# Kernel optimization log

Measured on AMD Instinct MI355X. Metric: run time of the kernel, lower is better.

The kernel has to match this reference:

```python
import jax, jax.numpy as jnp
import numpy as np

B, T, D = 8, 1024, 1024
F = 4 * D  # RWKV channel-mixing hidden size
EPS = 1e-3  # keras LayerNormalization default epsilon


def layer_norm(x, g, b):
    mu = jnp.mean(x, axis=-1, keepdims=True)
    var = jnp.var(x, axis=-1, keepdims=True)
    return (x - mu) * jax.lax.rsqrt(var + EPS) * g + b


def setup_inputs() -> dict:
    key = jax.random.key(0)
    ks = jax.random.split(key, 16)
    s = 0.02
    f32 = jnp.float32
    return {
        "x": jax.random.normal(ks[0], (B, T, D), f32),
        "att_x": jnp.zeros((B, D), f32),
        "att_a": jnp.zeros((B, D), f32),
        "att_b": jnp.zeros((B, D), f32),
        "att_p": jnp.zeros((B, D), f32),
        "ffn_x": jnp.zeros((B, D), f32),
        "ln1_g": jnp.ones((D,), f32),
        "ln1_b": jnp.zeros((D,), f32),
        "ln2_g": jnp.ones((D,), f32),
        "ln2_b": jnp.zeros((D,), f32),
        "tm_mix_k": jax.random.uniform(ks[1], (D,), f32),
        "tm_mix_v": jax.random.uniform(ks[2], (D,), f32),
        "tm_mix_r": jax.random.uniform(ks[3], (D,), f32),
        "tm_decay": jax.random.normal(ks[4], (D,), f32) * 0.1,
        "tm_first": jax.random.normal(ks[5], (D,), f32) * 0.1,
        "Wk": jax.random.normal(ks[6], (D, D), f32) * s,
        "Wv": jax.random.normal(ks[7], (D, D), f32) * s,
        "Wr": jax.random.normal(ks[8], (D, D), f32) * s,
        "Wo": jax.random.normal(ks[9], (D, D), f32) * s,
        "cm_mix_k": jax.random.uniform(ks[10], (D,), f32),
        "cm_mix_r": jax.random.uniform(ks[11], (D,), f32),
        "Ck": jax.random.normal(ks[12], (D, F), f32) * s,
        "Cr": jax.random.normal(ks[13], (D, D), f32) * s,
        "Cv": jax.random.normal(ks[14], (F, D), f32) * s,
    }


def _wkv_scan(k, v, aa, bb, pp, decay, first):
    # k, v: [B, T, D]; states: [B, D]. Numerically-stable RWKV-4 WKV recurrence.
    w = -jnp.exp(decay)  # per-channel decay, always negative

    def step(carry, kv):
        aa, bb, pp = carry
        k_t, v_t = kv
        ww = first + k_t
        p = jnp.maximum(pp, ww)
        e1 = jnp.exp(pp - p)
        e2 = jnp.exp(ww - p)
        wkv = (e1 * aa + e2 * v_t) / (e1 * bb + e2)
        ww2 = pp + w
        p2 = jnp.maximum(ww2, k_t)
        e1b = jnp.exp(ww2 - p2)
        e2b = jnp.exp(k_t - p2)
        return (e1b * aa + e2b * v_t, e1b * bb + e2b, p2), wkv

    kT = jnp.swapaxes(k, 0, 1)  # [T, B, D]
    vT = jnp.swapaxes(v, 0, 1)
    (aa, bb, pp), wkv = jax.lax.scan(step, (aa, bb, pp), (kT, vT))
    return jnp.swapaxes(wkv, 0, 1), aa, bb, pp


def reference(x, att_x, att_a, att_b, att_p, ffn_x,
              ln1_g, ln1_b, ln2_g, ln2_b,
              tm_mix_k, tm_mix_v, tm_mix_r, tm_decay, tm_first,
              Wk, Wv, Wr, Wo, cm_mix_k, cm_mix_r, Ck, Cr, Cv):
    # ---- time mixing (RWKV attention) on ln1(x) ----
    xn = layer_norm(x, ln1_g, ln1_b)  # [B, T, D]
    x_prev = jnp.concatenate([att_x[:, None, :], xn[:, :-1, :]], axis=1)  # token shift
    k = (xn * tm_mix_k + x_prev * (1.0 - tm_mix_k)) @ Wk
    v = (xn * tm_mix_v + x_prev * (1.0 - tm_mix_v)) @ Wv
    r = jax.nn.sigmoid((xn * tm_mix_r + x_prev * (1.0 - tm_mix_r)) @ Wr)
    wkv, aa, bb, pp = _wkv_scan(k, v, att_a, att_b, att_p, tm_decay, tm_first)
    x1 = x + (r * wkv) @ Wo  # residual

    # ---- channel mixing (FFN) on ln2(x1) ----
    xn2 = layer_norm(x1, ln2_g, ln2_b)
    xp = jnp.concatenate([ffn_x[:, None, :], xn2[:, :-1, :]], axis=1)
    kc = jnp.square(jax.nn.relu((xn2 * cm_mix_k + xp * (1.0 - cm_mix_k)) @ Ck))
    rc = jax.nn.sigmoid((xn2 * cm_mix_r + xp * (1.0 - cm_mix_r)) @ Cr)
    out = x1 + rc * (kc @ Cv)

    return (out, xn[:, -1, :], aa, bb, pp, xn2[:, -1, :])
```

## Files before the change

### kernel.cpp

```cpp
#include <hip/hip_runtime.h>

#define TT 1024
#define DD 1024
#define BB 8
#define FF 4096
#define MM (BB * TT)
#define CHL 32
#define NCH (TT / CHL)
#define NCHAN (BB * DD)

typedef unsigned short u16;
typedef unsigned int u32;

typedef __attribute__((ext_vector_type(8))) short short8;
typedef __attribute__((ext_vector_type(4))) float floatx4;

__device__ __forceinline__ u16 f2bf(float f) {
  u32 u = __float_as_uint(f);
  u32 r = (u + 0x7fffu + ((u >> 16) & 1u)) >> 16;
  return (u16)r;
}
__device__ __forceinline__ float bf2f(u16 h) { return __uint_as_float(((u32)h) << 16); }
__device__ __forceinline__ float sigmoidf_(float v) { return 1.0f / (1.0f + __expf(-v)); }

__global__ void transpose5_bf16(const float* __restrict__ w0, const float* __restrict__ w1,
                                const float* __restrict__ w2, const float* __restrict__ w3,
                                const float* __restrict__ w4, u16* __restrict__ outbase) {
  __shared__ float tile[32][33];
  const float* srcs[5] = {w0, w1, w2, w3, w4};
  const float* in = srcs[blockIdx.z];
  u16* out = outbase + (size_t)blockIdx.z * 1024 * 1024;
  int tx = threadIdx.x, ty = threadIdx.y;
  int n0 = blockIdx.x * 32, k0 = blockIdx.y * 32;
#pragma unroll
  for (int j = 0; j < 32; j += 8)
    tile[ty + j][tx] = in[(size_t)(k0 + ty + j) * 1024 + (n0 + tx)];
  __syncthreads();
#pragma unroll
  for (int j = 0; j < 32; j += 8)
    out[(size_t)(n0 + ty + j) * 1024 + (k0 + tx)] = f2bf(tile[tx][ty + j]);
}

__global__ void transpose_bf16(const float* __restrict__ in, u16* __restrict__ out, int K, int N) {
  __shared__ float tile[32][33];
  int tx = threadIdx.x, ty = threadIdx.y;
  int n0 = blockIdx.x * 32, k0 = blockIdx.y * 32;
#pragma unroll
  for (int j = 0; j < 32; j += 8)
    tile[ty + j][tx] = in[(size_t)(k0 + ty + j) * N + (n0 + tx)];
  __syncthreads();
#pragma unroll
  for (int j = 0; j < 32; j += 8)
    out[(size_t)(n0 + ty + j) * K + (k0 + tx)] = f2bf(tile[tx][ty + j]);
}

__global__ void ln1mix_kernel(const float* __restrict__ x, const float* __restrict__ attx,
                              const float* __restrict__ g, const float* __restrict__ be,
                              const float* __restrict__ mk, const float* __restrict__ mv,
                              const float* __restrict__ mr,
                              u16* __restrict__ xk, u16* __restrict__ xv, u16* __restrict__ xr,
                              float* __restrict__ xn_last) {
  int row = blockIdx.x, tid = threadIdx.x;
  int b = row >> 10, t = row & (TT - 1);
  float4 xc = ((const float4*)(x + (size_t)row * DD))[tid];
  float4 xp = (t == 0) ? ((const float4*)(attx + (size_t)b * DD))[tid]
                       : ((const float4*)(x + (size_t)(row - 1) * DD))[tid];
  float sc = xc.x + xc.y + xc.z + xc.w;
  float qc = xc.x * xc.x + xc.y * xc.y + xc.z * xc.z + xc.w * xc.w;
  float sp = xp.x + xp.y + xp.z + xp.w;
  float qp = xp.x * xp.x + xp.y * xp.y + xp.z * xp.z + xp.w * xp.w;
#pragma unroll
  for (int o = 32; o > 0; o >>= 1) {
    sc += __shfl_xor(sc, o); qc += __shfl_xor(qc, o);
    sp += __shfl_xor(sp, o); qp += __shfl_xor(qp, o);
  }
  __shared__ float red[4][4];
  int lane = tid & 63, wid = tid >> 6;
  if (lane == 0) { red[wid][0] = sc; red[wid][1] = qc; red[wid][2] = sp; red[wid][3] = qp; }
  __syncthreads();
  sc = red[0][0] + red[1][0] + red[2][0] + red[3][0];
  qc = red[0][1] + red[1][1] + red[2][1] + red[3][1];
  sp = red[0][2] + red[1][2] + red[2][2] + red[3][2];
  qp = red[0][3] + red[1][3] + red[2][3] + red[3][3];
  const float inv = 1.0f / (float)DD;
  float muc = sc * inv, varc = qc * inv - muc * muc;
  float rc = rsqrtf(varc + 1e-3f);
  float mup = sp * inv, varp = qp * inv - mup * mup;
  float rp = rsqrtf(varp + 1e-3f);
  float4 gg = ((const float4*)g)[tid];
  float4 bb = ((const float4*)be)[tid];
  float4 k4 = ((const float4*)mk)[tid];
  float4 v4 = ((const float4*)mv)[tid];
  float4 r4 = ((const float4*)mr)[tid];
  float xcv[4] = {xc.x, xc.y, xc.z, xc.w};
  float xpv[4] = {xp.x, xp.y, xp.z, xp.w};
  float gv[4] = {gg.x, gg.y, gg.z, gg.w};
  float bv[4] = {bb.x, bb.y, bb.z, bb.w};
  float kv[4] = {k4.x, k4.y, k4.z, k4.w};
  float vv[4] = {v4.x, v4.y, v4.z, v4.w};
  float rv[4] = {r4.x, r4.y, r4.z, r4.w};
  u16 ok[4], ov[4], orr[4];
  float nc[4];
#pragma unroll
  for (int i = 0; i < 4; i++) {
    nc[i] = (xcv[i] - muc) * rc * gv[i] + bv[i];
    float np = (t == 0) ? xpv[i] : ((xpv[i] - mup) * rp * gv[i] + bv[i]);
    ok[i] = f2bf(nc[i] * kv[i] + np * (1.0f - kv[i]));
    ov[i] = f2bf(nc[i] * vv[i] + np * (1.0f - vv[i]));
    orr[i] = f2bf(nc[i] * rv[i] + np * (1.0f - rv[i]));
  }
  size_t o4 = (size_t)row * (DD / 4) + tid;
  ((ushort4*)xk)[o4] = make_ushort4(ok[0], ok[1], ok[2], ok[3]);
  ((ushort4*)xv)[o4] = make_ushort4(ov[0], ov[1], ov[2], ov[3]);
  ((ushort4*)xr)[o4] = make_ushort4(orr[0], orr[1], orr[2], orr[3]);
  if (t == TT - 1)
    ((float4*)xn_last)[(size_t)b * (DD / 4) + tid] = make_float4(nc[0], nc[1], nc[2], nc[3]);
}

__global__ void ln2mix_kernel(const float* __restrict__ x1, const float* __restrict__ ffnx,
                              const float* __restrict__ g, const float* __restrict__ be,
                              const float* __restrict__ cmk, const float* __restrict__ cmr,
                              u16* __restrict__ xk2, u16* __restrict__ xr2,
                              float* __restrict__ xn2_last) {
  int row = blockIdx.x, tid = threadIdx.x;
  int b = row >> 10, t = row & (TT - 1);
  float4 xc = ((const float4*)(x1 + (size_t)row * DD))[tid];
  float4 xp = (t == 0) ? ((const float4*)(ffnx + (size_t)b * DD))[tid]
                       : ((const float4*)(x1 + (size_t)(row - 1) * DD))[tid];
  float sc = xc.x + xc.y + xc.z + xc.w;
  float qc = xc.x * xc.x + xc.y * xc.y + xc.z * xc.z + xc.w * xc.w;
  float sp = xp.x + xp.y + xp.z + xp.w;
  float qp = xp.x * xp.x + xp.y * xp.y + xp.z * xp.z + xp.w * xp.w;
#pragma unroll
  for (int o = 32; o > 0; o >>= 1) {
    sc += __shfl_xor(sc, o); qc += __shfl_xor(qc, o);
    sp += __shfl_xor(sp, o); qp += __shfl_xor(qp, o);
  }
  __shared__ float red[4][4];
  int lane = tid & 63, wid = tid >> 6;
  if (lane == 0) { red[wid][0] = sc; red[wid][1] = qc; red[wid][2] = sp; red[wid][3] = qp; }
  __syncthreads();
  sc = red[0][0] + red[1][0] + red[2][0] + red[3][0];
  qc = red[0][1] + red[1][1] + red[2][1] + red[3][1];
  sp = red[0][2] + red[1][2] + red[2][2] + red[3][2];
  qp = red[0][3] + red[1][3] + red[2][3] + red[3][3];
  const float inv = 1.0f / (float)DD;
  float muc = sc * inv, varc = qc * inv - muc * muc;
  float rc = rsqrtf(varc + 1e-3f);
  float mup = sp * inv, varp = qp * inv - mup * mup;
  float rp = rsqrtf(varp + 1e-3f);
  float4 gg = ((const float4*)g)[tid];
  float4 bb = ((const float4*)be)[tid];
  float4 k4 = ((const float4*)cmk)[tid];
  float4 r4 = ((const float4*)cmr)[tid];
  float xcv[4] = {xc.x, xc.y, xc.z, xc.w};
  float xpv[4] = {xp.x, xp.y, xp.z, xp.w};
  float gv[4] = {gg.x, gg.y, gg.z, gg.w};
  float bv[4] = {bb.x, bb.y, bb.z, bb.w};
  float kv[4] = {k4.x, k4.y, k4.z, k4.w};
  float rv[4] = {r4.x, r4.y, r4.z, r4.w};
  u16 ok[4], orr[4];
  float nc[4];
#pragma unroll
  for (int i = 0; i < 4; i++) {
    nc[i] = (xcv[i] - muc) * rc * gv[i] + bv[i];
    float np = (t == 0) ? xpv[i] : ((xpv[i] - mup) * rp * gv[i] + bv[i]);
    ok[i] = f2bf(nc[i] * kv[i] + np * (1.0f - kv[i]));
    orr[i] = f2bf(nc[i] * rv[i] + np * (1.0f - rv[i]));
  }
  size_t o4 = (size_t)row * (DD / 4) + tid;
  ((ushort4*)xk2)[o4] = make_ushort4(ok[0], ok[1], ok[2], ok[3]);
  ((ushort4*)xr2)[o4] = make_ushort4(orr[0], orr[1], orr[2], orr[3]);
  if (t == TT - 1)
    ((float4*)xn2_last)[(size_t)b * (DD / 4) + tid] = make_float4(nc[0], nc[1], nc[2], nc[3]);
}

__global__ void wkv_chunk_sum(const float* __restrict__ K, const float* __restrict__ V,
                              const float* __restrict__ decay,
                              float* __restrict__ sa, float* __restrict__ sb,
                              float* __restrict__ ps) {
  int f = blockIdx.x * 256 + threadIdx.x;
  int d = f & (DD - 1);
  int bc = f >> 10;
  int b = bc & (BB - 1);
  int chunk = bc >> 3;
  float w = -__expf(decay[d]);
  const float* kp = K + ((size_t)(b * TT + chunk * CHL)) * DD + d;
  const float* vp = V + ((size_t)(b * TT + chunk * CHL)) * DD + d;
  float aa = 0.0f, bb = 0.0f, pp = -1e30f;
#pragma unroll
  for (int j = 0; j < CHL; j++) {
    float kt = kp[(size_t)j * DD];
    float vt = vp[(size_t)j * DD];
    float ww2 = pp + w;
    float p2 = fmaxf(ww2, kt);
    float e1 = __expf(ww2 - p2);
    float e2 = __expf(kt - p2);
    aa = e1 * aa + e2 * vt;
    bb = e1 * bb + e2;
    pp = p2;
  }
  int ch = b * DD + d;
  size_t s = (size_t)chunk * NCHAN + ch;
  sa[s] = aa; sb[s] = bb; ps[s] = pp;
}

__global__ void wkv_chunk_scan(const float* __restrict__ sa, const float* __restrict__ sb,
                               const float* __restrict__ ps, const float* __restrict__ decay,
                               const float* __restrict__ aa0, const float* __restrict__ bb0,
                               const float* __restrict__ pp0,
                               float* __restrict__ pa, float* __restrict__ pb,
                               float* __restrict__ ppx,
                               float* __restrict__ aa_out, float* __restrict__ bb_out,
                               float* __restrict__ pp_out) {
  int ch = blockIdx.x * 256 + threadIdx.x;
  int d = ch & (DD - 1);
  float w = -__expf(decay[d]);
  float wL = (float)CHL * w;
  float aa = aa0[ch], bb = bb0[ch], pp = pp0[ch];
  float lsa[NCH], lsb[NCH], lps[NCH];
#pragma unroll
  for (int j = 0; j < NCH; j++) {
    size_t s = (size_t)j * NCHAN + ch;
    lsa[j] = sa[s]; lsb[j] = sb[s]; lps[j] = ps[s];
  }
#pragma unroll
  for (int j = 0; j < NCH; j++) {
    size_t s = (size_t)j * NCHAN + ch;
    pa[s] = aa; pb[s] = bb; ppx[s] = pp;
    float pw = pp + wL;
    float pn = fmaxf(pw, lps[j]);
    float e1 = __expf(pw - pn);
    float e2 = __expf(lps[j] - pn);
    aa = e1 * aa + e2 * lsa[j];
    bb = e1 * bb + e2 * lsb[j];
    pp = pn;
  }
  aa_out[ch] = aa; bb_out[ch] = bb; pp_out[ch] = pp;
}

__global__ void wkv_chunk_out(const float* __restrict__ K, const float* __restrict__ V,
                              const u16* __restrict__ sigr, const float* __restrict__ decay,
                              const float* __restrict__ first,
                              const float* __restrict__ pa, const float* __restrict__ pb,
                              const float* __restrict__ ppx, u16* __restrict__ rm) {
  int f = blockIdx.x * 256 + threadIdx.x;
  int d = f & (DD - 1);
  int bc = f >> 10;
  int b = bc & (BB - 1);
  int chunk = bc >> 3;
  float w = -__expf(decay[d]);
  float u = first[d];
  int ch = b * DD + d;
  size_t s = (size_t)chunk * NCHAN + ch;
  float aa = pa[s], bb = pb[s], pp = ppx[s];
  size_t base = ((size_t)(b * TT + chunk * CHL)) * DD + d;
  const float* kp = K + base;
  const float* vp = V + base;
  const u16* rp = sigr + base;
  u16* op = rm + base;
#pragma unroll
  for (int j = 0; j < CHL; j++) {
    float kt = kp[(size_t)j * DD];
    float vt = vp[(size_t)j * DD];
    float ww = u + kt;
    float p = fmaxf(pp, ww);
    float e1 = __expf(pp - p);
    float e2 = __expf(ww - p);
    float wkv = __fdividef(e1 * aa + e2 * vt, e1 * bb + e2);
    op[(size_t)j * DD] = f2bf(bf2f(rp[(size_t)j * DD]) * wkv);
    float ww2 = pp + w;
    float p2 = fmaxf(ww2, kt);
    float e1b = __expf(ww2 - p2);
    float e2b = __expf(kt - p2);
    aa = e1b * aa + e2b * vt;
    bb = e1b * bb + e2b;
    pp = p2;
  }
}


template <int MODE>
__launch_bounds__(256, 3)
__global__ void gemm_bt(const u16* __restrict__ A0, const u16* __restrict__ BT0,
                        const float* R1, const u16* R2,
                        void* C0, void* C1, void* C2, int M, int N, int K) {
  __shared__ u16 lA[128 * 64];
  __shared__ u16 lB[128 * 64];
  int tid = threadIdx.x;
  int lane = tid & 63;
  int wid = tid >> 6;
  int wy = wid >> 1, wx = wid & 1;

  const u16* A = A0;
  const u16* BT = BT0;
  void* Cout = C0;
  if (MODE == 5) {
    int z = blockIdx.z;
    A = A0 + (size_t)z * M * K;
    BT = BT0 + (size_t)z * N * K;
    Cout = (z == 0) ? C0 : (z == 1) ? C1 : C2;
  }

  int bx = blockIdx.x, by = blockIdx.y;
  {
    int flat = by * gridDim.x + bx;
    int j = flat >> 3;
    by = (flat & 7) * 8 + (j & 7);
    bx = j >> 3;
  }
  int m0 = by * 128, n0 = bx * 128;

  int rlo = lane & 15;
  int rr = tid >> 3;
  int cc = ((tid & 7) - rr) & 7;
  const u16* gA = A + (size_t)(m0 + rr) * K + cc * 8;
  const u16* gB = BT + (size_t)(n0 + rr) * K + cc * 8;
  u16* ldsA = lA + wid * 512;
  u16* ldsB = lB + wid * 512;
  size_t qstep = (size_t)32 * K;

  floatx4 acc[4][4];
#pragma unroll
  for (int mi = 0; mi < 4; mi++)
#pragma unroll
    for (int ni = 0; ni < 4; ni++)
#pragma unroll
      for (int e = 0; e < 4; e++) acc[mi][ni][e] = 0.0f;

  for (int kt = 0; kt < K; kt += 64) {
    __syncthreads();
#pragma unroll
    for (int q = 0; q < 4; q++) {
      __builtin_amdgcn_global_load_lds(gA + q * qstep + kt, ldsA + q * 2048, 16, 0, 0);
      __builtin_amdgcn_global_load_lds(gB + q * qstep + kt, ldsB + q * 2048, 16, 0, 0);
    }
    __syncthreads();
    short8 af[2][4], bfr[2][4];
#pragma unroll
    for (int s = 0; s < 2; s++) {
      int cbase = s * 4 + (lane >> 4);
#pragma unroll
      for (int mi = 0; mi < 4; mi++) {
        int row = wy * 64 + mi * 16 + rlo;
        af[s][mi] = *(const short8*)&lA[row * 64 + (((cbase + row) & 7) << 3)];
      }
#pragma unroll
      for (int ni = 0; ni < 4; ni++) {
        int row = wx * 64 + ni * 16 + rlo;
        bfr[s][ni] = *(const short8*)&lB[row * 64 + (((cbase + row) & 7) << 3)];
      }
    }
#pragma unroll
    for (int s = 0; s < 2; s++)
#pragma unroll
      for (int mi = 0; mi < 4; mi++)
#pragma unroll
        for (int ni = 0; ni < 4; ni++)
          acc[mi][ni] =
              __builtin_amdgcn_mfma_f32_16x16x32_bf16(af[s][mi], bfr[s][ni], acc[mi][ni], 0, 0, 0);
  }

  int rbase = (lane >> 4) * 4;
#pragma unroll
  for (int mi = 0; mi < 4; mi++) {
#pragma unroll
    for (int ni = 0; ni < 4; ni++) {
#pragma unroll
      for (int r = 0; r < 4; r++) {
        int row = m0 + wy * 64 + mi * 16 + rbase + r;
        int col = n0 + wx * 64 + ni * 16 + rlo;
        size_t idx = (size_t)row * N + col;
        float v = acc[mi][ni][r];
        if (MODE == 0) {
          ((float*)Cout)[idx] = v;
        } else if (MODE == 1) {
          ((u16*)Cout)[idx] = f2bf(sigmoidf_(v));
        } else if (MODE == 2) {
          float tpos = fmaxf(v, 0.0f);
          ((u16*)Cout)[idx] = f2bf(tpos * tpos);
        } else if (MODE == 3) {
          ((float*)Cout)[idx] = v + R1[idx];
        } else if (MODE == 4) {
          ((float*)Cout)[idx] = R1[idx] + bf2f(R2[idx]) * v;
        } else {
          if (blockIdx.z == 2)
            ((u16*)Cout)[idx] = f2bf(sigmoidf_(v));
          else
            ((float*)Cout)[idx] = v;
        }
      }
    }
  }
}

extern "C" void kernel_launch(void* const* d_in, const int* in_sizes, int n_in,
                              void* d_out, int out_size, void* d_ws, size_t ws_size,
                              hipStream_t stream) {
  const float* x    = (const float*)d_in[0];
  const float* attx = (const float*)d_in[1];
  const float* aa0  = (const float*)d_in[2];
  const float* bb0  = (const float*)d_in[3];
  const float* pp0  = (const float*)d_in[4];
  const float* ffnx = (const float*)d_in[5];
  const float* ln1g = (const float*)d_in[6];
  const float* ln1b = (const float*)d_in[7];
  const float* ln2g = (const float*)d_in[8];
  const float* ln2b = (const float*)d_in[9];
  const float* mk   = (const float*)d_in[10];
  const float* mv   = (const float*)d_in[11];
  const float* mr   = (const float*)d_in[12];
  const float* decay= (const float*)d_in[13];
  const float* first= (const float*)d_in[14];
  const float* Wk   = (const float*)d_in[15];
  const float* Wv   = (const float*)d_in[16];
  const float* Wr   = (const float*)d_in[17];
  const float* Wo   = (const float*)d_in[18];
  const float* cmk  = (const float*)d_in[19];
  const float* cmr  = (const float*)d_in[20];
  const float* Ck   = (const float*)d_in[21];
  const float* Cr   = (const float*)d_in[22];
  const float* Cv   = (const float*)d_in[23];

  float* out      = (float*)d_out;
  float* xn_last  = out + (size_t)BB * TT * DD;
  float* aa_out   = xn_last + BB * DD;
  float* bb_out   = aa_out + BB * DD;
  float* pp_out   = bb_out + BB * DD;
  float* xn2_last = pp_out + BB * DD;
  float* x1 = out;

  char* ws = (char*)d_ws;
  const size_t MB = 1024ull * 1024ull;
  u16* WT5   = (u16*)(ws + 0 * MB);
  u16* WkT   = WT5;
  u16* WoT   = (u16*)(ws + 6 * MB);
  u16* CrT   = (u16*)(ws + 8 * MB);
  u16* CkT   = (u16*)(ws + 10 * MB);
  u16* CvT   = (u16*)(ws + 18 * MB);
  u16* xk    = (u16*)(ws + 26 * MB);
  u16* xv    = (u16*)(ws + 42 * MB);
  u16* xr    = (u16*)(ws + 58 * MB);
  float* kbuf= (float*)(ws + 74 * MB);
  float* vbuf= (float*)(ws + 106 * MB);
  u16* sigr  = (u16*)(ws + 138 * MB);
  float* sab = (float*)(ws + 154 * MB);
  float* sbb = (float*)(ws + 155 * MB);
  float* psb = (float*)(ws + 156 * MB);
  float* pab = (float*)(ws + 157 * MB);
  float* pbb = (float*)(ws + 158 * MB);
  float* ppb = (float*)(ws + 159 * MB);
  u16* rmb   = (u16*)(ws + 26 * MB);
  u16* xk2   = (u16*)(ws + 26 * MB);
  u16* xr2   = (u16*)(ws + 42 * MB);
  u16* sigr2 = (u16*)(ws + 58 * MB);
  u16* kc    = (u16*)(ws + 74 * MB);

  dim3 tb32(32, 8);
  transpose5_bf16<<<dim3(32, 32, 5), tb32, 0, stream>>>(Wk, Wv, Wr, Wo, Cr, WT5);
  transpose_bf16<<<dim3(128, 32), tb32, 0, stream>>>(Ck, CkT, 1024, 4096);
  transpose_bf16<<<dim3(32, 128), tb32, 0, stream>>>(Cv, CvT, 4096, 1024);

  ln1mix_kernel<<<MM, 256, 0, stream>>>(x, attx, ln1g, ln1b, mk, mv, mr, xk, xv, xr, xn_last);

  gemm_bt<5><<<dim3(8, 64, 3), 256, 0, stream>>>(xk, WkT, nullptr, nullptr,
                                                 kbuf, vbuf, sigr, MM, 1024, 1024);

  wkv_chunk_sum<<<NCHAN * NCH / 256, 256, 0, stream>>>(kbuf, vbuf, decay, sab, sbb, psb);
  wkv_chunk_scan<<<NCHAN / 256, 256, 0, stream>>>(sab, sbb, psb, decay, aa0, bb0, pp0,
                                                  pab, pbb, ppb, aa_out, bb_out, pp_out);
  wkv_chunk_out<<<NCHAN * NCH / 256, 256, 0, stream>>>(kbuf, vbuf, sigr, decay, first,
                                                       pab, pbb, ppb, rmb);

  gemm_bt<3><<<dim3(8, 64), 256, 0, stream>>>(rmb, WoT, x, nullptr, x1, nullptr, nullptr,
                                              MM, 1024, 1024);

  ln2mix_kernel<<<MM, 256, 0, stream>>>(x1, ffnx, ln2g, ln2b, cmk, cmr, xk2, xr2, xn2_last);

  gemm_bt<2><<<dim3(32, 64), 256, 0, stream>>>(xk2, CkT, nullptr, nullptr, kc, nullptr, nullptr,
                                               MM, 4096, 1024);
  gemm_bt<1><<<dim3(8, 64), 256, 0, stream>>>(xr2, CrT, nullptr, nullptr, sigr2, nullptr, nullptr,
                                              MM, 1024, 1024);
  gemm_bt<4><<<dim3(8, 64), 256, 0, stream>>>(kc, CvT, x1, sigr2, out, nullptr, nullptr,
                                              MM, 1024, 4096);
}
```

Measured before the change: 511.8 us.

## Store k/v in bf16 and fuse Ck and Cr GEMMs into one launch

The projection GEMM now writes k and v as bf16 instead of fp32, halving the traffic the WKV chunk kernels read. The Ck and Cr channel-mix GEMMs merge into one launch over a concatenated transposed weight buffer, and each block picks its A matrix and epilogue by column range. Launch bounds rise to 4 blocks per SM to raise occupancy. The cost is lower precision on k/v before the exponential recurrence, and possible register pressure from the tighter bounds.

New measurement: 502.8 us. No clear change (-1.8%).

```diff
diff --git a/kernel.cpp b/kernel.cpp
--- a/kernel.cpp
+++ b/kernel.cpp
@@ -25,11 +25,12 @@
 
 __global__ void transpose5_bf16(const float* __restrict__ w0, const float* __restrict__ w1,
                                 const float* __restrict__ w2, const float* __restrict__ w3,
-                                const float* __restrict__ w4, u16* __restrict__ outbase) {
+                                const float* __restrict__ w4,
+                                u16* __restrict__ out4, u16* __restrict__ crdst) {
   __shared__ float tile[32][33];
   const float* srcs[5] = {w0, w1, w2, w3, w4};
   const float* in = srcs[blockIdx.z];
-  u16* out = outbase + (size_t)blockIdx.z * 1024 * 1024;
+  u16* out = (blockIdx.z == 4) ? crdst : out4 + (size_t)blockIdx.z * 1024 * 1024;
   int tx = threadIdx.x, ty = threadIdx.y;
   int n0 = blockIdx.x * 32, k0 = blockIdx.y * 32;
 #pragma unroll
@@ -175,7 +176,7 @@
     ((float4*)xn2_last)[(size_t)b * (DD / 4) + tid] = make_float4(nc[0], nc[1], nc[2], nc[3]);
 }
 
-__global__ void wkv_chunk_sum(const float* __restrict__ K, const float* __restrict__ V,
+__global__ void wkv_chunk_sum(const u16* __restrict__ K, const u16* __restrict__ V,
                               const float* __restrict__ decay,
                               float* __restrict__ sa, float* __restrict__ sb,
                               float* __restrict__ ps) {
@@ -185,13 +186,13 @@
   int b = bc & (BB - 1);
   int chunk = bc >> 3;
   float w = -__expf(decay[d]);
-  const float* kp = K + ((size_t)(b * TT + chunk * CHL)) * DD + d;
-  const float* vp = V + ((size_t)(b * TT + chunk * CHL)) * DD + d;
+  const u16* kp = K + ((size_t)(b * TT + chunk * CHL)) * DD + d;
+  const u16* vp = V + ((size_t)(b * TT + chunk * CHL)) * DD + d;
   float aa = 0.0f, bb = 0.0f, pp = -1e30f;
 #pragma unroll
   for (int j = 0; j < CHL; j++) {
-    float kt = kp[(size_t)j * DD];
-    float vt = vp[(size_t)j * DD];
+    float kt = bf2f(kp[(size_t)j * DD]);
+    float vt = bf2f(vp[(size_t)j * DD]);
     float ww2 = pp + w;
     float p2 = fmaxf(ww2, kt);
     float e1 = __expf(ww2 - p2);
@@ -239,7 +240,7 @@
   aa_out[ch] = aa; bb_out[ch] = bb; pp_out[ch] = pp;
 }
 
-__global__ void wkv_chunk_out(const float* __restrict__ K, const float* __restrict__ V,
+__global__ void wkv_chunk_out(const u16* __restrict__ K, const u16* __restrict__ V,
                               const u16* __restrict__ sigr, const float* __restrict__ decay,
                               const float* __restrict__ first,
                               const float* __restrict__ pa, const float* __restrict__ pb,
@@ -255,14 +256,14 @@
   size_t s = (size_t)chunk * NCHAN + ch;
   float aa = pa[s], bb = pb[s], pp = ppx[s];
   size_t base = ((size_t)(b * TT + chunk * CHL)) * DD + d;
-  const float* kp = K + base;
-  const float* vp = V + base;
+  const u16* kp = K + base;
+  const u16* vp = V + base;
   const u16* rp = sigr + base;
   u16* op = rm + base;
 #pragma unroll
   for (int j = 0; j < CHL; j++) {
-    float kt = kp[(size_t)j * DD];
-    float vt = vp[(size_t)j * DD];
+    float kt = bf2f(kp[(size_t)j * DD]);
+    float vt = bf2f(vp[(size_t)j * DD]);
     float ww = u + kt;
     float p = fmaxf(pp, ww);
     float e1 = __expf(pp - p);
@@ -281,10 +282,11 @@
 
 
 template <int MODE>
-__launch_bounds__(256, 3)
-__global__ void gemm_bt(const u16* __restrict__ A0, const u16* __restrict__ BT0,
+__launch_bounds__(256, 4)
+__global__ void gemm_bt(const u16* __restrict__ A0, const u16* __restrict__ A1,
+                        const u16* __restrict__ BT0,
                         const float* R1, const u16* R2,
-                        void* C0, void* C1, void* C2, int M, int N, int K) {
+                        void* C0, void* C1, int M, int N, int K) {
   __shared__ u16 lA[128 * 64];
   __shared__ u16 lB[128 * 64];
   int tid = threadIdx.x;
@@ -299,7 +301,7 @@
     int z = blockIdx.z;
     A = A0 + (size_t)z * M * K;
     BT = BT0 + (size_t)z * N * K;
-    Cout = (z == 0) ? C0 : (z == 1) ? C1 : C2;
+    Cout = (void*)((u16*)C0 + (size_t)z * M * N);
   }
 
   int bx = blockIdx.x, by = blockIdx.y;
@@ -310,6 +312,12 @@
     bx = j >> 3;
   }
   int m0 = by * 128, n0 = bx * 128;
+
+  bool isCr = false;
+  if (MODE == 6) {
+    isCr = (bx >= 32);
+    A = isCr ? A1 : A0;
+  }
 
   int rlo = lane & 15;
   int rr = tid >> 3;
@@ -370,24 +378,23 @@
       for (int r = 0; r < 4; r++) {
         int row = m0 + wy * 64 + mi * 16 + rbase + r;
         int col = n0 + wx * 64 + ni * 16 + rlo;
-        size_t idx = (size_t)row * N + col;
         float v = acc[mi][ni][r];
-        if (MODE == 0) {
-          ((float*)Cout)[idx] = v;
-        } else if (MODE == 1) {
-          ((u16*)Cout)[idx] = f2bf(sigmoidf_(v));
-        } else if (MODE == 2) {
-          float tpos = fmaxf(v, 0.0f);
-          ((u16*)Cout)[idx] = f2bf(tpos * tpos);
-        } else if (MODE == 3) {
-          ((float*)Cout)[idx] = v + R1[idx];
-        } else if (MODE == 4) {
-          ((float*)Cout)[idx] = R1[idx] + bf2f(R2[idx]) * v;
+        if (MODE == 6) {
+          if (!isCr) {
+            float tpos = fmaxf(v, 0.0f);
+            ((u16*)C0)[(size_t)row * 4096 + col] = f2bf(tpos * tpos);
+          } else {
+            ((u16*)C1)[(size_t)row * 1024 + (col - 4096)] = f2bf(sigmoidf_(v));
+          }
         } else {
-          if (blockIdx.z == 2)
-            ((u16*)Cout)[idx] = f2bf(sigmoidf_(v));
-          else
-            ((float*)Cout)[idx] = v;
+          size_t idx = (size_t)row * N + col;
+          if (MODE == 3) {
+            ((float*)Cout)[idx] = v + R1[idx];
+          } else if (MODE == 4) {
+            ((float*)Cout)[idx] = R1[idx] + bf2f(R2[idx]) * v;
+          } else if (MODE == 5) {
+            ((u16*)Cout)[idx] = (blockIdx.z == 2) ? f2bf(sigmoidf_(v)) : f2bf(v);
+          }
         }
       }
     }
@@ -432,24 +439,24 @@
 
   char* ws = (char*)d_ws;
   const size_t MB = 1024ull * 1024ull;
-  u16* WT5   = (u16*)(ws + 0 * MB);
-  u16* WkT   = WT5;
-  u16* WoT   = (u16*)(ws + 6 * MB);
-  u16* CrT   = (u16*)(ws + 8 * MB);
-  u16* CkT   = (u16*)(ws + 10 * MB);
+  u16* WT4   = (u16*)(ws + 0 * MB);
+  u16* WkT   = WT4;
+  u16* WoT   = WT4 + 3u * 1024 * 1024;
+  u16* CkCrT = (u16*)(ws + 8 * MB);
+  u16* CrTd  = CkCrT + (size_t)4096 * 1024;
   u16* CvT   = (u16*)(ws + 18 * MB);
   u16* xk    = (u16*)(ws + 26 * MB);
   u16* xv    = (u16*)(ws + 42 * MB);
   u16* xr    = (u16*)(ws + 58 * MB);
-  float* kbuf= (float*)(ws + 74 * MB);
-  float* vbuf= (float*)(ws + 106 * MB);
-  u16* sigr  = (u16*)(ws + 138 * MB);
-  float* sab = (float*)(ws + 154 * MB);
-  float* sbb = (float*)(ws + 155 * MB);
-  float* psb = (float*)(ws + 156 * MB);
-  float* pab = (float*)(ws + 157 * MB);
-  float* pbb = (float*)(ws + 158 * MB);
-  float* ppb = (float*)(ws + 159 * MB);
+  u16* kbuf  = (u16*)(ws + 74 * MB);
+  u16* vbuf  = (u16*)(ws + 90 * MB);
+  u16* sigr  = (u16*)(ws + 106 * MB);
+  float* sab = (float*)(ws + 122 * MB);
+  float* sbb = (float*)(ws + 123 * MB);
+  float* psb = (float*)(ws + 124 * MB);
+  float* pab = (float*)(ws + 125 * MB);
+  float* pbb = (float*)(ws + 126 * MB);
+  float* ppb = (float*)(ws + 127 * MB);
   u16* rmb   = (u16*)(ws + 26 * MB);
   u16* xk2   = (u16*)(ws + 26 * MB);
   u16* xr2   = (u16*)(ws + 42 * MB);
@@ -457,14 +464,14 @@
   u16* kc    = (u16*)(ws + 74 * MB);
 
   dim3 tb32(32, 8);
-  transpose5_bf16<<<dim3(32, 32, 5), tb32, 0, stream>>>(Wk, Wv, Wr, Wo, Cr, WT5);
-  transpose_bf16<<<dim3(128, 32), tb32, 0, stream>>>(Ck, CkT, 1024, 4096);
+  transpose5_bf16<<<dim3(32, 32, 5), tb32, 0, stream>>>(Wk, Wv, Wr, Wo, Cr, WT4, CrTd);
+  transpose_bf16<<<dim3(128, 32), tb32, 0, stream>>>(Ck, CkCrT, 1024, 4096);
   transpose_bf16<<<dim3(32, 128), tb32, 0, stream>>>(Cv, CvT, 4096, 1024);
 
   ln1mix_kernel<<<MM, 256, 0, stream>>>(x, attx, ln1g, ln1b, mk, mv, mr, xk, xv, xr, xn_last);
 
-  gemm_bt<5><<<dim3(8, 64, 3), 256, 0, stream>>>(xk, WkT, nullptr, nullptr,
-                                                 kbuf, vbuf, sigr, MM, 1024, 1024);
+  gemm_bt<5><<<dim3(8, 64, 3), 256, 0, stream>>>(xk, nullptr, WkT, nullptr, nullptr,
+                                                 kbuf, nullptr, MM, 1024, 1024);
 
   wkv_chunk_sum<<<NCHAN * NCH / 256, 256, 0, stream>>>(kbuf, vbuf, decay, sab, sbb, psb);
   wkv_chunk_scan<<<NCHAN / 256, 256, 0, stream>>>(sab, sbb, psb, decay, aa0, bb0, pp0,
@@ -472,15 +479,14 @@
   wkv_chunk_out<<<NCHAN * NCH / 256, 256, 0, stream>>>(kbuf, vbuf, sigr, decay, first,
                                                        pab, pbb, ppb, rmb);
 
-  gemm_bt<3><<<dim3(8, 64), 256, 0, stream>>>(rmb, WoT, x, nullptr, x1, nullptr, nullptr,
-                                              MM, 1024, 1024);
+  gemm_bt<3><<<dim3(8, 64), 256, 0, stream>>>(rmb, nullptr, WoT, x, nullptr,
+                                              x1, nullptr, MM, 1024, 1024);
 
   ln2mix_kernel<<<MM, 256, 0, stream>>>(x1, ffnx, ln2g, ln2b, cmk, cmr, xk2, xr2, xn2_last);
 
-  gemm_bt<2><<<dim3(32, 64), 256, 0, stream>>>(xk2, CkT, nullptr, nullptr, kc, nullptr, nullptr,
-                                               MM, 4096, 1024);
-  gemm_bt<1><<<dim3(8, 64), 256, 0, stream>>>(xr2, CrT, nullptr, nullptr, sigr2, nullptr, nullptr,
-                                              MM, 1024, 1024);
-  gemm_bt<4><<<dim3(8, 64), 256, 0, stream>>>(kc, CvT, x1, sigr2, out, nullptr, nullptr,
-                                              MM, 1024, 4096);
-}
+  gemm_bt<6><<<dim3(40, 64), 256, 0, stream>>>(xk2, xr2, CkCrT, nullptr, nullptr,
+                                               kc, sigr2, MM, 5120, 1024);
+
+  gemm_bt<4><<<dim3(8, 64), 256, 0, stream>>>(kc, nullptr, CvT, x1, sigr2,
+                                              out, nullptr, MM, 1024, 4096);
+}
```
